# Kernel optimization log

Measured on AMD Instinct MI355X. Metric: run time of the kernel, lower is better.

## Reference

```python
import jax, jax.numpy as jnp
from jax import lax
import numpy as np

DN = ('NDHWC', 'DHWIO', 'NDHWC')

def conv3d(x, w, b, stride=1):
    return lax.conv_general_dilated(x, w, (stride,) * 3, 'SAME', dimension_numbers=DN) + b

def convT3d(x, w, b, stride=2):
    return lax.conv_transpose(x, w, (stride,) * 3, 'SAME', dimension_numbers=DN) + b

def prelu(x, a):
    return jnp.where(x > 0, x, a * x)

def bn(x, g, be, m, v):
    # keras BatchNormalization, inference mode, epsilon=1e-3
    return (x - m) * g * lax.rsqrt(v + 1e-3) + be

def res_unit(x, c1w, c1b, c2w, c2b, g, be, m, v, a):
    # VQVAEResidualUnit: relu(x + PReLU(BN(conv2(swish(conv1(x))))))
    h = jax.nn.swish(conv3d(x, c1w, c1b))
    h = prelu(bn(conv3d(h, c2w, c2b), g, be, m, v), a)
    return jax.nn.relu(x + h)

def _forward(x, ec0_w, ec0_b, er0_c1w, er0_c1b, er0_c2w, er0_c2b, er0_g, er0_be, er0_m, er0_v, er0_a, ec1_w, ec1_b, er1_c1w, er1_c1b, er1_c2w, er1_c2b, er1_g, er1_be, er1_m, er1_v, er1_a, eo_w, eo_b, eo_a, codebook, dc0_w, dc0_b, dc0_a, dr0_c1w, dr0_c1b, dr0_c2w, dr0_c2b, dr0_g, dr0_be, dr0_m, dr0_v, dr0_a, du0_w, du0_b, dr1_c1w, dr1_c1b, dr1_c2w, dr1_c2b, dr1_g, dr1_be, dr1_m, dr1_v, dr1_a, du1_w, du1_b):
    # ----- Encoder -----
    h = jax.nn.relu(conv3d(x, ec0_w, ec0_b, stride=2))   # [B,64,64,64,64]
    h = res_unit(h, er0_c1w, er0_c1b, er0_c2w, er0_c2b, er0_g, er0_be, er0_m, er0_v, er0_a)
    h = jax.nn.relu(conv3d(h, ec1_w, ec1_b, stride=2))   # [B,32,32,32,128]
    h = res_unit(h, er1_c1w, er1_c1b, er1_c2w, er1_c2b, er1_g, er1_be, er1_m, er1_v, er1_a)
    z = prelu(conv3d(h, eo_w, eo_b), eo_a)               # [B,32,32,32,64] latent
    # ----- NSVQ (inference: hard codebook lookup) -----
    D = z.shape[-1]
    flat = z.reshape(-1, D)                              # [N, 64], N = B*32^3
    dist = (flat * flat).sum(1, keepdims=True) + (codebook * codebook).sum(1) - 2.0 * (flat @ codebook.T)  # [N, K]
    idx = jnp.argmin(dist, axis=1)
    zq = codebook[idx].reshape(z.shape)
    K = codebook.shape[0]
    p = jnp.zeros((K,), jnp.float32).at[idx].add(1.0) / flat.shape[0]
    perplexity = jnp.exp(-jnp.sum(p * jnp.log(p + 1e-12)))
    # ----- Decoder -----
    h = prelu(conv3d(zq, dc0_w, dc0_b), dc0_a)           # [B,32,32,32,128]
    h = res_unit(h, dr0_c1w, dr0_c1b, dr0_c2w, dr0_c2b, dr0_g, dr0_be, dr0_m, dr0_v, dr0_a)
    h = jax.nn.relu(convT3d(h, du0_w, du0_b))            # [B,64,64,64,64]
    h = res_unit(h, dr1_c1w, dr1_c1b, dr1_c2w, dr1_c2b, dr1_g, dr1_be, dr1_m, dr1_v, dr1_a)
    recon = convT3d(h, du1_w, du1_b)                     # [B,128,128,128,1]
    return recon, perplexity

def setup_inputs() -> dict:
    key = jax.random.key(0)
    ks = iter(jax.random.split(key, 40))
    nrm = lambda *s: jax.random.normal(next(ks), s, jnp.float32) * 0.05
    def ru(pfx, c):
        return {pfx + '_c1w': nrm(3, 3, 3, c, c), pfx + '_c1b': jnp.zeros((c,), jnp.float32),
                pfx + '_c2w': nrm(3, 3, 3, c, c), pfx + '_c2b': jnp.zeros((c,), jnp.float32),
                pfx + '_g': jnp.ones((c,), jnp.float32), pfx + '_be': jnp.zeros((c,), jnp.float32),
                pfx + '_m': jnp.zeros((c,), jnp.float32), pfx + '_v': jnp.ones((c,), jnp.float32),
                pfx + '_a': jnp.full((c,), 0.25, jnp.float32)}
    C0, C1, D, K = 64, 128, 64, 512
    inp = {'x': jax.random.normal(next(ks), (2, 128, 128, 128, 1), jnp.float32)}
    inp.update(ec0_w=nrm(4, 4, 4, 1, C0), ec0_b=jnp.zeros((C0,), jnp.float32))
    inp.update(ru('er0', C0))
    inp.update(ec1_w=nrm(4, 4, 4, C0, C1), ec1_b=jnp.zeros((C1,), jnp.float32))
    inp.update(ru('er1', C1))
    inp.update(eo_w=nrm(3, 3, 3, C1, D), eo_b=jnp.zeros((D,), jnp.float32), eo_a=jnp.full((D,), 0.25, jnp.float32))
    inp.update(codebook=jax.random.uniform(next(ks), (K, D), jnp.float32, -1.0, 1.0) * np.sqrt(6.0 / D).astype(np.float32))
    inp.update(dc0_w=nrm(3, 3, 3, D, C1), dc0_b=jnp.zeros((C1,), jnp.float32), dc0_a=jnp.full((C1,), 0.25, jnp.float32))
    inp.update(ru('dr0', C1))
    inp.update(du0_w=nrm(4, 4, 4, C1, C0), du0_b=jnp.zeros((C0,), jnp.float32))
    inp.update(ru('dr1', C0))
    inp.update(du1_w=nrm(4, 4, 4, C0, 1), du1_b=jnp.zeros((1,), jnp.float32))
    return inp

def reference(x, ec0_w, ec0_b, er0_c1w, er0_c1b, er0_c2w, er0_c2b, er0_g, er0_be, er0_m, er0_v, er0_a, ec1_w, ec1_b, er1_c1w, er1_c1b, er1_c2w, er1_c2b, er1_g, er1_be, er1_m, er1_v, er1_a, eo_w, eo_b, eo_a, codebook, dc0_w, dc0_b, dc0_a, dr0_c1w, dr0_c1b, dr0_c2w, dr0_c2b, dr0_g, dr0_be, dr0_m, dr0_v, dr0_a, du0_w, du0_b, dr1_c1w, dr1_c1b, dr1_c2w, dr1_c2b, dr1_g, dr1_be, dr1_m, dr1_v, dr1_a, du1_w, du1_b):
    return _forward(x, ec0_w, ec0_b, er0_c1w, er0_c1b, er0_c2w, er0_c2b, er0_g, er0_be, er0_m, er0_v, er0_a, ec1_w, ec1_b, er1_c1w, er1_c1b, er1_c2w, er1_c2b, er1_g, er1_be, er1_m, er1_v, er1_a, eo_w, eo_b, eo_a, codebook, dc0_w, dc0_b, dc0_a, dr0_c1w, dr0_c1b, dr0_c2w, dr0_c2b, dr0_g, dr0_be, dr0_m, dr0_v, dr0_a, du0_w, du0_b, dr1_c1w, dr1_c1b, dr1_c2w, dr1_c2b, dr1_g, dr1_be, dr1_m, dr1_v, dr1_a, du1_w, du1_b)
```

## Files before the change

kernel.cpp:

```cpp
#include <hip/hip_runtime.h>
#include <cstdint>


typedef unsigned short bf16_t;
typedef __attribute__((ext_vector_type(8)))  short s8b;
typedef __attribute__((ext_vector_type(16))) float f32x16;

__device__ __forceinline__ float b2f(bf16_t u) { return __uint_as_float((unsigned)u << 16); }
__device__ __forceinline__ bf16_t f2b(float f) {
    unsigned x = __float_as_uint(f);
    return (bf16_t)((x + 0x7FFFu + ((x >> 16) & 1u)) >> 16);
}

__device__ __forceinline__ void split3s(float v, unsigned short& h,
                                        unsigned short& m, unsigned short& l)
{
    const unsigned uv = __float_as_uint(v);
    const float fh = __uint_as_float(uv & 0xFFFF0000u);
    const float r1 = v - fh;
    const unsigned u1 = __float_as_uint(r1);
    const float fm = __uint_as_float(u1 & 0xFFFF0000u);
    const float r2 = r1 - fm;
    h = (unsigned short)(uv >> 16);
    m = (unsigned short)(u1 >> 16);
    l = (unsigned short)(__float_as_uint(r2) >> 16);
}

__device__ __forceinline__ int wdst(int tap, int ci_, int co_, int ci, int co)
{
    const int ks = ci_ >> 4, half = (ci_ >> 3) & 1, j = ci_ & 7;
    return (((tap * (ci >> 4) + ks) * 2 + half) * co + co_) * 8 + j;
}

__global__ __launch_bounds__(256)
void wprep3(const float* __restrict__ w, bf16_t* __restrict__ h,
            bf16_t* __restrict__ m, bf16_t* __restrict__ l,
            int ci, int co, int n)
{
    const int i = blockIdx.x * 256 + threadIdx.x;
    if (i >= n) return;
    const int co_ = i % co;
    const int ci_ = (i / co) % ci;
    const int tap = i / (co * ci);
    const int dst = wdst(tap, ci_, co_, ci, co);
    unsigned short hh, mm, ll2;
    split3s(w[i], hh, mm, ll2);
    h[dst] = hh; m[dst] = mm; l[dst] = ll2;
}

__global__ __launch_bounds__(256)
void wprep_split(const float* __restrict__ w, bf16_t* __restrict__ hi,
                 bf16_t* __restrict__ lo, int ci, int co, int n)
{
    const int i = blockIdx.x * 256 + threadIdx.x;
    if (i >= n) return;
    const int co_ = i % co;
    const int ci_ = (i / co) % ci;
    const int tap = i / (co * ci);
    const float v = w[i];
    const int dst = wdst(tap, ci_, co_, ci, co);
    const bf16_t h = f2b(v);
    hi[dst] = h;
    lo[dst] = f2b(v - b2f(h));
}

template<int CIN, int COUT, int SD, int NWC, int EPI>
__global__ __launch_bounds__((SD / 32) * NWC * 64)
void conv3e(const float* __restrict__ xf,
            const bf16_t* __restrict__ wh, const bf16_t* __restrict__ wm,
            const bf16_t* __restrict__ wl,
            const float* __restrict__ bias,
            const float* __restrict__ g, const float* __restrict__ be,
            const float* __restrict__ mn, const float* __restrict__ vr,
            const float* __restrict__ al,
            const float* skf, float* __restrict__ of)
{
    constexpr int NT = (SD / 32) * NWC * 64;
    constexpr int LP = (SD * CIN) / (4 * NT);
    constexpr int KS = CIN / 16;
    __shared__ bf16_t lh[(SD + 2) * CIN], lm[(SD + 2) * CIN], ll[(SD + 2) * CIN];

    const int tid  = threadIdx.x;
    const int lane = tid & 63;
    const int wid  = tid >> 6;
    const int wn   = wid % NWC, wm2 = wid / NWC;
    const int half = lane >> 5, ln = lane & 31;
    const int w    = wm2 * 32 + ln;
    const int nwg  = gridDim.x;
    const int bid  = (blockIdx.x & 7) * (nwg >> 3) + (blockIdx.x >> 3);
    const int h    = bid % SD;
    const int d    = (bid / SD) % SD;
    const int b    = bid / (SD * SD);
    const int cout = wn * 32 + ln;

    int pz[9], py[9], pt[9], np = 0;
    for (int kd = 0; kd < 3; ++kd) {
        const int iz = d + kd - 1;
        if ((unsigned)iz >= (unsigned)SD) continue;
        for (int kh = 0; kh < 3; ++kh) {
            const int iy = h + kh - 1;
            if ((unsigned)iy >= (unsigned)SD) continue;
            pz[np] = iz; py[np] = iy; pt[np] = (kd * 3 + kh) * 3; ++np;
        }
    }

    f32x16 accA, accB;
#pragma unroll
    for (int i = 0; i < 16; ++i) { accA[i] = 0.f; accB[i] = 0.f; }

    for (int i = tid; i < CIN / 2; i += NT) {
        const int pv = (i < CIN / 4) ? 0 : (SD + 1);
        const int ch = (i % (CIN / 4)) * 4;
        const int bo = ((pv * CIN + ch) * 2) ^ ((pv & 7) << 4);
        const ushort4 z4 = make_ushort4(0, 0, 0, 0);
        *reinterpret_cast<ushort4*>((char*)&lh[0] + bo) = z4;
        *reinterpret_cast<ushort4*>((char*)&lm[0] + bo) = z4;
        *reinterpret_cast<ushort4*>((char*)&ll[0] + bo) = z4;
    }

    float4 rg[LP];
    auto loadrow = [&](int iz, int iy) {
        const float* src = xf + ((size_t)((b * SD + iz) * SD + iy)) * SD * CIN;
#pragma unroll
        for (int j = 0; j < LP; ++j)
            rg[j] = *reinterpret_cast<const float4*>(src + (size_t)(tid + j * NT) * 4);
    };
    auto writerow = [&]() {
#pragma unroll
        for (int j = 0; j < LP; ++j) {
            const int idx = (tid + j * NT) * 4;
            const int pv = idx / CIN + 1, ch = idx % CIN;
            ushort4 h4, m4, l4;
            split3s(rg[j].x, h4.x, m4.x, l4.x);
            split3s(rg[j].y, h4.y, m4.y, l4.y);
            split3s(rg[j].z, h4.z, m4.z, l4.z);
            split3s(rg[j].w, h4.w, m4.w, l4.w);
            const int bo = ((pv * CIN + ch) * 2) ^ ((pv & 7) << 4);
            *reinterpret_cast<ushort4*>((char*)&lh[0] + bo) = h4;
            *reinterpret_cast<ushort4*>((char*)&lm[0] + bo) = m4;
            *reinterpret_cast<ushort4*>((char*)&ll[0] + bo) = l4;
        }
    };

    loadrow(pz[0], py[0]);
    writerow();
    __syncthreads();
#pragma unroll 1
    for (int i = 0; i < np; ++i) {
        if (i + 1 < np) loadrow(pz[i + 1], py[i + 1]);
#pragma unroll
        for (int kw = 0; kw < 3; ++kw) {
            const int tap = pt[i] + kw;
            const int pv = w + kw;
#pragma unroll
            for (int ks = 0; ks < KS; ++ks) {
                const int bo = ((pv * CIN + half * 8 + ks * 16) * 2) ^ ((pv & 7) << 4);
                const s8b ah  = *reinterpret_cast<const s8b*>((const char*)&lh[0] + bo);
                const s8b am  = *reinterpret_cast<const s8b*>((const char*)&lm[0] + bo);
                const s8b al3 = *reinterpret_cast<const s8b*>((const char*)&ll[0] + bo);
                const size_t wb = ((size_t)((tap * KS + ks) * 2 + half) * COUT + cout) * 8;
                const s8b bh = *reinterpret_cast<const s8b*>(wh + wb);
                const s8b bm = *reinterpret_cast<const s8b*>(wm + wb);
                const s8b bl = *reinterpret_cast<const s8b*>(wl + wb);
                accA = __builtin_amdgcn_mfma_f32_32x32x16_bf16(ah, bh, accA, 0, 0, 0);
                accB = __builtin_amdgcn_mfma_f32_32x32x16_bf16(ah, bm, accB, 0, 0, 0);
                accA = __builtin_amdgcn_mfma_f32_32x32x16_bf16(am, bh, accA, 0, 0, 0);
                accB = __builtin_amdgcn_mfma_f32_32x32x16_bf16(am, bm, accB, 0, 0, 0);
                accA = __builtin_amdgcn_mfma_f32_32x32x16_bf16(al3, bh, accA, 0, 0, 0);
                accB = __builtin_amdgcn_mfma_f32_32x32x16_bf16(ah, bl, accB, 0, 0, 0);
            }
        }
        if (i + 1 < np) {
            __syncthreads();
            writerow();
            __syncthreads();
        }
    }

    const size_t outrow = ((size_t)((b * SD + d) * SD + h)) * SD;
    const float bv = bias[cout];
    float sc = 0.f, mm = 0.f, bb2 = 0.f, aa = 0.f;
    if constexpr (EPI == 3) {
        sc = g[cout] * (1.0f / sqrtf(vr[cout] + 1e-3f));
        mm = mn[cout]; bb2 = be[cout]; aa = al[cout];
    }
    if constexpr (EPI == 2) aa = al[cout];
#pragma unroll
    for (int r = 0; r < 16; ++r) {
        const int rl = (r & 3) + 8 * (r >> 2) + 4 * half;
        const size_t oe = (outrow + wm2 * 32 + rl) * COUT + cout;
        float y = accA[r] + accB[r] + bv;
        if constexpr (EPI == 0) y = fmaxf(y, 0.f);
        else if constexpr (EPI == 1) y = y / (1.f + expf(-y));
        else if constexpr (EPI == 2) y = y > 0.f ? y : aa * y;
        else {
            float t2 = (y - mm) * sc + bb2;
            t2 = t2 > 0.f ? t2 : aa * t2;
            y = fmaxf(skf[oe] + t2, 0.f);
        }
        of[oe] = y;
    }
}

__global__ __launch_bounds__(256)
void convs2e(const float* __restrict__ xf,
             const bf16_t* __restrict__ wh, const bf16_t* __restrict__ wm,
             const bf16_t* __restrict__ wl,
             const float* __restrict__ bias, float* __restrict__ of)
{
    constexpr int NT = 256, LP = (64 * 64) / (4 * NT);
    __shared__ bf16_t lh[66 * 64], lm[66 * 64], ll[66 * 64];

    const int tid  = threadIdx.x;
    const int lane = tid & 63;
    const int wn   = tid >> 6;
    const int half = lane >> 5, ln = lane & 31;
    const int nwg  = gridDim.x;
    const int bid  = (blockIdx.x & 7) * (nwg >> 3) + (blockIdx.x >> 3);
    const int h    = bid % 32;
    const int d    = (bid / 32) % 32;
    const int b    = bid / 1024;
    const int cout = wn * 32 + ln;

    int pz[16], py[16], pt[16], np = 0;
    for (int kd = 0; kd < 4; ++kd) {
        const int iz = 2 * d + kd - 1;
        if ((unsigned)iz >= 64u) continue;
        for (int kh = 0; kh < 4; ++kh) {
            const int iy = 2 * h + kh - 1;
            if ((unsigned)iy >= 64u) continue;
            pz[np] = iz; py[np] = iy; pt[np] = (kd * 4 + kh) * 4; ++np;
        }
    }

    f32x16 accA, accB;
#pragma unroll
    for (int i = 0; i < 16; ++i) { accA[i] = 0.f; accB[i] = 0.f; }

    for (int i = tid; i < 32; i += NT) {
        const int pv = (i < 16) ? 0 : 65;
        const int ch = (i % 16) * 4;
        const int bo = ((pv * 64 + ch) * 2) ^ ((pv & 7) << 4);
        const ushort4 z4 = make_ushort4(0, 0, 0, 0);
        *reinterpret_cast<ushort4*>((char*)&lh[0] + bo) = z4;
        *reinterpret_cast<ushort4*>((char*)&lm[0] + bo) = z4;
        *reinterpret_cast<ushort4*>((char*)&ll[0] + bo) = z4;
    }

    float4 rg[LP];
    auto loadrow = [&](int iz, int iy) {
        const float* src = xf + ((size_t)((b * 64 + iz) * 64 + iy)) * 64 * 64;
#pragma unroll
        for (int j = 0; j < LP; ++j)
            rg[j] = *reinterpret_cast<const float4*>(src + (size_t)(tid + j * NT) * 4);
    };
    auto writerow = [&]() {
#pragma unroll
        for (int j = 0; j < LP; ++j) {
            const int idx = (tid + j * NT) * 4;
            const int pv = idx / 64 + 1, ch = idx % 64;
            ushort4 h4, m4, l4;
            split3s(rg[j].x, h4.x, m4.x, l4.x);
            split3s(rg[j].y, h4.y, m4.y, l4.y);
            split3s(rg[j].z, h4.z, m4.z, l4.z);
            split3s(rg[j].w, h4.w, m4.w, l4.w);
            const int bo = ((pv * 64 + ch) * 2) ^ ((pv & 7) << 4);
            *reinterpret_cast<ushort4*>((char*)&lh[0] + bo) = h4;
            *reinterpret_cast<ushort4*>((char*)&lm[0] + bo) = m4;
            *reinterpret_cast<ushort4*>((char*)&ll[0] + bo) = l4;
        }
    };

    loadrow(pz[0], py[0]);
    writerow();
    __syncthreads();
#pragma unroll 1
    for (int i = 0; i < np; ++i) {
        if (i + 1 < np) loadrow(pz[i + 1], py[i + 1]);
#pragma unroll
        for (int kw = 0; kw < 4; ++kw) {
            const int tap = pt[i] + kw;
            const int pv = 2 * ln + kw;
#pragma unroll
            for (int ks = 0; ks < 4; ++ks) {
                const int bo = ((pv * 64 + half * 8 + ks * 16) * 2) ^ ((pv & 7) << 4);
                const s8b ah  = *reinterpret_cast<const s8b*>((const char*)&lh[0] + bo);
                const s8b am  = *reinterpret_cast<const s8b*>((const char*)&lm[0] + bo);
                const s8b al3 = *reinterpret_cast<const s8b*>((const char*)&ll[0] + bo);
                const size_t wb = ((size_t)((tap * 4 + ks) * 2 + half) * 128 + cout) * 8;
                const s8b bh = *reinterpret_cast<const s8b*>(wh + wb);
                const s8b bm = *reinterpret_cast<const s8b*>(wm + wb);
                const s8b bl = *reinterpret_cast<const s8b*>(wl + wb);
                accA = __builtin_amdgcn_mfma_f32_32x32x16_bf16(ah, bh, accA, 0, 0, 0);
                accB = __builtin_amdgcn_mfma_f32_32x32x16_bf16(ah, bm, accB, 0, 0, 0);
                accA = __builtin_amdgcn_mfma_f32_32x32x16_bf16(am, bh, accA, 0, 0, 0);
                accB = __builtin_amdgcn_mfma_f32_32x32x16_bf16(am, bm, accB, 0, 0, 0);
                accA = __builtin_amdgcn_mfma_f32_32x32x16_bf16(al3, bh, accA, 0, 0, 0);
                accB = __builtin_amdgcn_mfma_f32_32x32x16_bf16(ah, bl, accB, 0, 0, 0);
            }
        }
        if (i + 1 < np) {
            __syncthreads();
            writerow();
            __syncthreads();
        }
    }

    const size_t outrow = ((size_t)((b * 32 + d) * 32 + h)) * 32;
    const float bv = bias[cout];
#pragma unroll
    for (int r = 0; r < 16; ++r) {
        const int rl = (r & 3) + 8 * (r >> 2) + 4 * half;
        const size_t oe = (outrow + rl) * 128 + cout;
        of[oe] = fmaxf(accA[r] + accB[r] + bv, 0.f);
    }
}

template<int CIN, int COUT, int SD, int NWC, int EPI>
__global__ __launch_bounds__((SD / 32) * NWC * 64)
void conv3d(const bf16_t* __restrict__ xh, const bf16_t* __restrict__ xl,
            const bf16_t* __restrict__ wh, const bf16_t* __restrict__ wl,
            const float* __restrict__ bias,
            const float* __restrict__ g, const float* __restrict__ be,
            const float* __restrict__ mn, const float* __restrict__ vr,
            const float* __restrict__ al,
            const bf16_t* skh, const bf16_t* skl,
            bf16_t* oh, bf16_t* ol)
{
    constexpr int NT = (SD / 32) * NWC * 64;
    constexpr int LP = (SD * CIN) / (4 * NT);
    constexpr int KS = CIN / 16;
    __shared__ bf16_t lh[(SD + 2) * CIN], ll[(SD + 2) * CIN];

    const int tid  = threadIdx.x;
    const int lane = tid & 63;
    const int wid  = tid >> 6;
    const int wn   = wid % NWC, wm2 = wid / NWC;
    const int half = lane >> 5, ln = lane & 31;
    const int w    = wm2 * 32 + ln;
    const int nwg  = gridDim.x;
    const int bid  = (blockIdx.x & 7) * (nwg >> 3) + (blockIdx.x >> 3);
    const int h    = bid % SD;
    const int d    = (bid / SD) % SD;
    const int b    = bid / (SD * SD);
    const int cout = wn * 32 + ln;

    int pz[9], py[9], pt[9], np = 0;
    for (int kd = 0; kd < 3; ++kd) {
        const int iz = d + kd - 1;
        if ((unsigned)iz >= (unsigned)SD) continue;
        for (int kh = 0; kh < 3; ++kh) {
            const int iy = h + kh - 1;
            if ((unsigned)iy >= (unsigned)SD) continue;
            pz[np] = iz; py[np] = iy; pt[np] = (kd * 3 + kh) * 3; ++np;
        }
    }

    f32x16 accA, accB;
#pragma unroll
    for (int i = 0; i < 16; ++i) { accA[i] = 0.f; accB[i] = 0.f; }

    for (int i = tid; i < CIN / 2; i += NT) {
        const int pv = (i < CIN / 4) ? 0 : (SD + 1);
        const int ch = (i % (CIN / 4)) * 4;
        const int bo = ((pv * CIN + ch) * 2) ^ ((pv & 7) << 4);
        const ushort4 z4 = make_ushort4(0, 0, 0, 0);
        *reinterpret_cast<ushort4*>((char*)&lh[0] + bo) = z4;
        *reinterpret_cast<ushort4*>((char*)&ll[0] + bo) = z4;
    }

    ushort4 rh[LP], rl2a[LP];
    auto loadrow = [&](int iz, int iy) {
        const size_t rb = ((size_t)((b * SD + iz) * SD + iy)) * SD * CIN;
#pragma unroll
        for (int j = 0; j < LP; ++j) {
            const int idx = (tid + j * NT) * 4;
            rh[j]   = *reinterpret_cast<const ushort4*>(xh + rb + idx);
            rl2a[j] = *reinterpret_cast<const ushort4*>(xl + rb + idx);
        }
    };
    auto writerow = [&]() {
#pragma unroll
        for (int j = 0; j < LP; ++j) {
            const int idx = (tid + j * NT) * 4;
            const int pv = idx / CIN + 1, ch = idx % CIN;
            const int bo = ((pv * CIN + ch) * 2) ^ ((pv & 7) << 4);
            *reinterpret_cast<ushort4*>((char*)&lh[0] + bo) = rh[j];
            *reinterpret_cast<ushort4*>((char*)&ll[0] + bo) = rl2a[j];
        }
    };

    loadrow(pz[0], py[0]);
    writerow();
    __syncthreads();
#pragma unroll 1
    for (int i = 0; i < np; ++i) {
        if (i + 1 < np) loadrow(pz[i + 1], py[i + 1]);
#pragma unroll
        for (int kw = 0; kw < 3; ++kw) {
            const int tap = pt[i] + kw;
            const int pv = w + kw;
#pragma unroll
            for (int ks = 0; ks < KS; ++ks) {
                const int bo = ((pv * CIN + half * 8 + ks * 16) * 2) ^ ((pv & 7) << 4);
                const s8b ah  = *reinterpret_cast<const s8b*>((const char*)&lh[0] + bo);
                const s8b al2 = *reinterpret_cast<const s8b*>((const char*)&ll[0] + bo);
                const size_t wb = ((size_t)((tap * KS + ks) * 2 + half) * COUT + cout) * 8;
                const s8b bh = *reinterpret_cast<const s8b*>(wh + wb);
                const s8b bl = *reinterpret_cast<const s8b*>(wl + wb);
                accA = __builtin_amdgcn_mfma_f32_32x32x16_bf16(ah, bh, accA, 0, 0, 0);
                accB = __builtin_amdgcn_mfma_f32_32x32x16_bf16(al2, bh, accB, 0, 0, 0);
                accB = __builtin_amdgcn_mfma_f32_32x32x16_bf16(ah, bl, accB, 0, 0, 0);
            }
        }
        if (i + 1 < np) {
            __syncthreads();
            writerow();
            __syncthreads();
        }
    }

    const size_t outrow = ((size_t)((b * SD + d) * SD + h)) * SD;
    const float bv = bias[cout];
    float sc = 0.f, mm = 0.f, bb2 = 0.f, aa = 0.f;
    if constexpr (EPI == 3) {
        sc = g[cout] * (1.0f / sqrtf(vr[cout] + 1e-3f));
        mm = mn[cout]; bb2 = be[cout]; aa = al[cout];
    }
    if constexpr (EPI == 2) aa = al[cout];
#pragma unroll
    for (int r = 0; r < 16; ++r) {
        const int rl3 = (r & 3) + 8 * (r >> 2) + 4 * half;
        const size_t oe = (outrow + wm2 * 32 + rl3) * COUT + cout;
        float y = accA[r] + accB[r] + bv;
        if constexpr (EPI == 0) y = fmaxf(y, 0.f);
        else if constexpr (EPI == 1) y = y / (1.f + expf(-y));
        else if constexpr (EPI == 2) y = y > 0.f ? y : aa * y;
        else {
            float t2 = (y - mm) * sc + bb2;
            t2 = t2 > 0.f ? t2 : aa * t2;
            float sv = b2f(skh[oe]) + b2f(skl[oe]);
            y = fmaxf(sv + t2, 0.f);
        }
        const bf16_t hh = f2b(y);
        oh[oe] = hh;
        ol[oe] = f2b(y - b2f(hh));
    }
}

__global__ __launch_bounds__(256)
void convTm(const bf16_t* __restrict__ xh, const bf16_t* __restrict__ xl,
            const bf16_t* __restrict__ wh, const bf16_t* __restrict__ wl,
            const float* __restrict__ bias,
            bf16_t* __restrict__ oh, bf16_t* __restrict__ ol)
{
    constexpr int NT = 256, LP = (32 * 128) / (4 * NT);
    __shared__ bf16_t lh[34 * 128], ll[34 * 128];

    const int tid  = threadIdx.x;
    const int lane = tid & 63;
    const int wid  = tid >> 6;
    const int wn   = wid & 1, p = wid >> 1;
    const int half = lane >> 5, ln = lane & 31;
    const int nwg  = gridDim.x;
    const int bid  = (blockIdx.x & 7) * (nwg >> 3) + (blockIdx.x >> 3);
    const int ohh  = bid % 64;
    const int od   = (bid / 64) % 64;
    const int b    = bid / 4096;
    const int pd = od & 1, dz = od >> 1;
    const int ph = ohh & 1, hy = ohh >> 1;
    const int cout = wn * 32 + ln;

    int pz[4], py[4], pt[4], np = 0;
    for (int jd = 0; jd < 2; ++jd) {
        const int kd = pd + 2 * jd;
        const int iz = dz + pd - 1 + jd;
        if ((unsigned)iz >= 32u) continue;
        for (int jh = 0; jh < 2; ++jh) {
            const int kh = ph + 2 * jh;
            const int iy = hy + ph - 1 + jh;
            if ((unsigned)iy >= 32u) continue;
            pz[np] = iz; py[np] = iy; pt[np] = (kd * 4 + kh) * 4; ++np;
        }
    }

    f32x16 accA, accB;
#pragma unroll
    for (int i = 0; i < 16; ++i) { accA[i] = 0.0f; accB[i] = 0.0f; }

    for (int i = tid; i < 64; i += NT) {
        const int pv = (i < 32) ? 0 : 33;
        const int ch = (i % 32) * 4;
        const int bo = ((pv * 128 + ch) * 2) ^ ((pv & 7) << 4);
        const ushort4 z4 = make_ushort4(0, 0, 0, 0);
        *reinterpret_cast<ushort4*>((char*)&lh[0] + bo) = z4;
        *reinterpret_cast<ushort4*>((char*)&ll[0] + bo) = z4;
    }

    ushort4 rh[LP], rl2a[LP];
    auto loadrow = [&](int iz, int iy) {
        const size_t rb = ((size_t)((b * 32 + iz) * 32 + iy)) * 32 * 128;
#pragma unroll
        for (int j = 0; j < LP; ++j) {
            const int idx = (tid + j * NT) * 4;
            rh[j]   = *reinterpret_cast<const ushort4*>(xh + rb + idx);
            rl2a[j] = *reinterpret_cast<const ushort4*>(xl + rb + idx);
        }
    };
    auto writerow = [&]() {
#pragma unroll
        for (int j = 0; j < LP; ++j) {
            const int idx = (tid + j * NT) * 4;
            const int pv = idx / 128 + 1, ch = idx % 128;
            const int bo = ((pv * 128 + ch) * 2) ^ ((pv & 7) << 4);
            *reinterpret_cast<ushort4*>((char*)&lh[0] + bo) = rh[j];
            *reinterpret_cast<ushort4*>((char*)&ll[0] + bo) = rl2a[j];
        }
    };

    loadrow(pz[0], py[0]);
    writerow();
    __syncthreads();
#pragma unroll 1
    for (int i = 0; i < np; ++i) {
        if (i + 1 < np) loadrow(pz[i + 1], py[i + 1]);
#pragma unroll
        for (int jw = 0; jw < 2; ++jw) {
            const int kw = p + 2 * jw;
            const int tap = pt[i] + kw;
            const int pv = ln + p + jw;
#pragma unroll
            for (int ks = 0; ks < 8; ++ks) {
                const int bo = ((pv * 128 + half * 8 + ks * 16) * 2) ^ ((pv & 7) << 4);
                const s8b a  = *reinterpret_cast<const s8b*>((const char*)&lh[0] + bo);
                const s8b a2 = *reinterpret_cast<const s8b*>((const char*)&ll[0] + bo);
                const size_t wb = ((size_t)((tap * 8 + ks) * 2 + half) * 64 + cout) * 8;
                const s8b bb = *reinterpret_cast<const s8b*>(wh + wb);
                const s8b b2 = *reinterpret_cast<const s8b*>(wl + wb);
                accA = __builtin_amdgcn_mfma_f32_32x32x16_bf16(a, bb, accA, 0, 0, 0);
                accB = __builtin_amdgcn_mfma_f32_32x32x16_bf16(a2, bb, accB, 0, 0, 0);
                accB = __builtin_amdgcn_mfma_f32_32x32x16_bf16(a, b2, accB, 0, 0, 0);
            }
        }
        if (i + 1 < np) {
            __syncthreads();
            writerow();
            __syncthreads();
        }
    }

    const float bv = bias[cout];
#pragma unroll
    for (int r = 0; r < 16; ++r) {
        const int rl3 = (r & 3) + 8 * (r >> 2) + 4 * half;
        const int ow = 2 * rl3 + p;
        const size_t oe = (((size_t)((b * 64 + od) * 64 + ohh)) * 64 + ow) * 64 + cout;
        const float y = fmaxf(accA[r] + accB[r] + bv, 0.f);
        const bf16_t hh = f2b(y);
        oh[oe] = hh;
        ol[oe] = f2b(y - b2f(hh));
    }
}

__global__ __launch_bounds__(128)
void conv_ec0m(const float* __restrict__ x,
               const bf16_t* __restrict__ wh, const bf16_t* __restrict__ wm,
               const bf16_t* __restrict__ wl,
               const float* __restrict__ bias, float* __restrict__ of)
{
    __shared__ bf16_t lh[16 * 132], lm[16 * 132], ll[16 * 132];

    const int tid  = threadIdx.x;
    const int lane = tid & 63;
    const int wm2  = tid >> 6;
    const int half = lane >> 5, ln = lane & 31;
    const int w    = wm2 * 32 + ln;
    const int nwg  = gridDim.x;
    const int bid  = (blockIdx.x & 7) * (nwg >> 3) + (blockIdx.x >> 3);
    const int h    = bid % 64;
    const int d    = (bid / 64) % 64;
    const int b    = bid / 4096;

    for (int i = tid; i < 16 * 132; i += 128) {
        const int row = i / 132, col = i % 132;
        const int kd = row >> 2, kh = row & 3;
        const int iz = 2 * d + kd - 1, iy = 2 * h + kh - 1;
        const int ix = col - 1;
        float v = 0.f;
        if ((unsigned)iz < 128u && (unsigned)iy < 128u &&
            (unsigned)ix < 128u && col < 130)
            v = x[(size_t)((b * 128 + iz) * 128 + iy) * 128 + ix];
        unsigned short hh, mm2, ll2;
        split3s(v, hh, mm2, ll2);
        lh[i] = hh; lm[i] = mm2; ll[i] = ll2;
    }
    __syncthreads();

    f32x16 accA[2], accB[2];
#pragma unroll
    for (int i = 0; i < 16; ++i) {
        accA[0][i] = 0.f; accA[1][i] = 0.f;
        accB[0][i] = 0.f; accB[1][i] = 0.f;
    }

#pragma unroll
    for (int ks = 0; ks < 4; ++ks) {
        const int row0 = ks * 4 + 2 * half;
        const int i0 = row0 * 132 + 2 * w;
        const int i1 = i0 + 132;
        s8b ah, am, al3;
        {
            uint* ap = (uint*)&ah;
            ap[0] = *(const uint*)&lh[i0]; ap[1] = *(const uint*)&lh[i0 + 2];
            ap[2] = *(const uint*)&lh[i1]; ap[3] = *(const uint*)&lh[i1 + 2];
        }
        {
            uint* ap = (uint*)&am;
            ap[0] = *(const uint*)&lm[i0]; ap[1] = *(const uint*)&lm[i0 + 2];
            ap[2] = *(const uint*)&lm[i1]; ap[3] = *(const uint*)&lm[i1 + 2];
        }
        {
            uint* ap = (uint*)&al3;
            ap[0] = *(const uint*)&ll[i0]; ap[1] = *(const uint*)&ll[i0 + 2];
            ap[2] = *(const uint*)&ll[i1]; ap[3] = *(const uint*)&ll[i1 + 2];
        }
        const size_t wb0 = ((size_t)(ks * 2 + half) * 64 + ln) * 8;
#pragma unroll
        for (int n2 = 0; n2 < 2; ++n2) {
            const size_t wb = wb0 + n2 * 256;
            const s8b bh = *reinterpret_cast<const s8b*>(wh + wb);
            const s8b bm = *reinterpret_cast<const s8b*>(wm + wb);
            const s8b bl = *reinterpret_cast<const s8b*>(wl + wb);
            accA[n2] = __builtin_amdgcn_mfma_f32_32x32x16_bf16(ah, bh, accA[n2], 0, 0, 0);
            accB[n2] = __builtin_amdgcn_mfma_f32_32x32x16_bf16(ah, bm, accB[n2], 0, 0, 0);
            accA[n2] = __builtin_amdgcn_mfma_f32_32x32x16_bf16(am, bh, accA[n2], 0, 0, 0);
            accB[n2] = __builtin_amdgcn_mfma_f32_32x32x16_bf16(am, bm, accB[n2], 0, 0, 0);
            accA[n2] = __builtin_amdgcn_mfma_f32_32x32x16_bf16(al3, bh, accA[n2], 0, 0, 0);
            accB[n2] = __builtin_amdgcn_mfma_f32_32x32x16_bf16(ah, bl, accB[n2], 0, 0, 0);
        }
    }

    const size_t outrow = ((size_t)((b * 64 + d) * 64 + h)) * 64;
#pragma unroll
    for (int n2 = 0; n2 < 2; ++n2) {
        const int cout = n2 * 32 + ln;
        const float bv = bias[cout];
#pragma unroll
        for (int r = 0; r < 16; ++r) {
            const int rl3 = (r & 3) + 8 * (r >> 2) + 4 * half;
            const size_t oe = (outrow + wm2 * 32 + rl3) * 64 + cout;
            of[oe] = fmaxf(accA[n2][r] + accB[n2][r] + bv, 0.f);
        }
    }
}

__global__ __launch_bounds__(256)
void convT_du1w(const bf16_t* __restrict__ inh, const bf16_t* __restrict__ inl,
                const float* __restrict__ wt, const float* __restrict__ bias,
                float* __restrict__ out)
{
    const int lane = threadIdx.x & 63;
    const int wv   = blockIdx.x * 4 + (threadIdx.x >> 6);
    const size_t obase = (size_t)wv * 16;
    const int ow0 = (int)(obase % 128);
    size_t rem = obase / 128;
    const int ohh = (int)(rem % 128); rem /= 128;
    const int od  = (int)(rem % 128); rem /= 128;
    const int b   = (int)rem;
    const int pd = od & 1, dz = od >> 1;
    const int ph = ohh & 1, hy = ohh >> 1;
    const int wx0 = ow0 >> 1;

    float acc[16];
#pragma unroll
    for (int o = 0; o < 16; ++o) acc[o] = 0.f;

#pragma unroll
    for (int jd = 0; jd < 2; ++jd) {
        const int kd = pd + 2 * jd;
        const int iz = dz + pd - 1 + jd;
        if ((unsigned)iz >= 64u) continue;
#pragma unroll
        for (int jh = 0; jh < 2; ++jh) {
            const int kh = ph + 2 * jh;
            const int iy = hy + ph - 1 + jh;
            if ((unsigned)iy >= 64u) continue;
            const size_t rbase = ((size_t)((b * 64 + iz) * 64 + iy)) * 64;
            float wv4[4];
#pragma unroll
            for (int kw = 0; kw < 4; ++kw)
                wv4[kw] = wt[(size_t)((kd * 4 + kh) * 4 + kw) * 64 + lane];
            float v[10];
#pragma unroll
            for (int t = 0; t < 10; ++t) {
                const int ix = wx0 - 1 + t;
                if ((unsigned)ix < 64u) {
                    const size_t a = (rbase + ix) * 64 + lane;
                    v[t] = b2f(inh[a]) + b2f(inl[a]);
                } else {
                    v[t] = 0.f;
                }
            }
#pragma unroll
            for (int o = 0; o < 16; ++o) {
                const int pw = o & 1;
                const int t0 = (o >> 1) + pw;
                acc[o] = fmaf(v[t0],     wv4[pw],     acc[o]);
                acc[o] = fmaf(v[t0 + 1], wv4[pw + 2], acc[o]);
            }
        }
    }

    const float b0 = bias[0];
#pragma unroll
    for (int o = 0; o < 16; ++o) {
        float s = acc[o];
        s += __shfl_xor(s, 1);
        s += __shfl_xor(s, 2);
        s += __shfl_xor(s, 4);
        s += __shfl_xor(s, 8);
        s += __shfl_xor(s, 16);
        s += __shfl_xor(s, 32);
        if (lane == 0) out[obase + o] = s + b0;
    }
}

__global__ void zero512(float* __restrict__ p) { p[threadIdx.x] = 0.0f; }

__global__ void vq_cnorm(const float* __restrict__ cb, float* __restrict__ cnorm)
{
    const int k = blockIdx.x * 64 + threadIdx.x;
    float s = 0.0f;
    for (int ci = 0; ci < 64; ++ci) { const float c = cb[k * 64 + ci]; s = fmaf(c, c, s); }
    cnorm[k] = s;
}

__global__ __launch_bounds__(256)
void vq_assign(const float* __restrict__ z, const float* __restrict__ cb,
               const float* __restrict__ cnorm, int* __restrict__ idx,
               float* __restrict__ hist, int N)
{
    const int n = blockIdx.x * 256 + threadIdx.x;
    const float4* zp = reinterpret_cast<const float4*>(z + (size_t)n * 64);
    float4 zv[16];
    float z2 = 0.0f;
#pragma unroll
    for (int i = 0; i < 16; ++i) {
        zv[i] = zp[i];
        z2 += zv[i].x * zv[i].x + zv[i].y * zv[i].y + zv[i].z * zv[i].z + zv[i].w * zv[i].w;
    }
    float best = 3.4e38f;
    int bi = 0;
#pragma unroll 1
    for (int k = 0; k < 512; k += 4) {
        float dot0 = 0.f, dot1 = 0.f, dot2 = 0.f, dot3 = 0.f;
        const float4* c0 = reinterpret_cast<const float4*>(cb + (size_t)(k + 0) * 64);
        const float4* c1 = reinterpret_cast<const float4*>(cb + (size_t)(k + 1) * 64);
        const float4* c2 = reinterpret_cast<const float4*>(cb + (size_t)(k + 2) * 64);
        const float4* c3 = reinterpret_cast<const float4*>(cb + (size_t)(k + 3) * 64);
#pragma unroll
        for (int i = 0; i < 16; ++i) {
            const float4 zi = zv[i];
            const float4 a0 = c0[i];
            const float4 a1 = c1[i];
            const float4 a2 = c2[i];
            const float4 a3 = c3[i];
            dot0 += zi.x * a0.x + zi.y * a0.y + zi.z * a0.z + zi.w * a0.w;
            dot1 += zi.x * a1.x + zi.y * a1.y + zi.z * a1.z + zi.w * a1.w;
            dot2 += zi.x * a2.x + zi.y * a2.y + zi.z * a2.z + zi.w * a2.w;
            dot3 += zi.x * a3.x + zi.y * a3.y + zi.z * a3.z + zi.w * a3.w;
        }
        const float d0 = z2 + cnorm[k + 0] - 2.0f * dot0;
        const float d1 = z2 + cnorm[k + 1] - 2.0f * dot1;
        const float d2 = z2 + cnorm[k + 2] - 2.0f * dot2;
        const float d3 = z2 + cnorm[k + 3] - 2.0f * dot3;
        if (d0 < best) { best = d0; bi = k + 0; }
        if (d1 < best) { best = d1; bi = k + 1; }
        if (d2 < best) { best = d2; bi = k + 2; }
        if (d3 < best) { best = d3; bi = k + 3; }
    }
    idx[n] = bi;
    atomicAdd(&hist[bi], 1.0f);
}

__global__ __launch_bounds__(256)
void vq_gather_split(const float* __restrict__ cb, const int* __restrict__ idx,
                     bf16_t* __restrict__ zh, bf16_t* __restrict__ zl)
{
    const int gid = blockIdx.x * 256 + threadIdx.x;
    const int n = gid >> 4, c4 = gid & 15;
    const int k = idx[n];
    const float4 c = reinterpret_cast<const float4*>(cb)[k * 16 + c4];
    ushort4 h, l;
    h.x = f2b(c.x); l.x = f2b(c.x - b2f(h.x));
    h.y = f2b(c.y); l.y = f2b(c.y - b2f(h.y));
    h.z = f2b(c.z); l.z = f2b(c.z - b2f(h.z));
    h.w = f2b(c.w); l.w = f2b(c.w - b2f(h.w));
    reinterpret_cast<ushort4*>(zh)[gid] = h;
    reinterpret_cast<ushort4*>(zl)[gid] = l;
}

__global__ __launch_bounds__(512)
void perplexity_k(const float* __restrict__ hist, float* __restrict__ out, float invN)
{
    __shared__ float red[512];
    const int t = threadIdx.x;
    const float p = hist[t] * invN;
    red[t] = p * logf(p + 1e-12f);
    __syncthreads();
    for (int s = 256; s > 0; s >>= 1) {
        if (t < s) red[t] += red[t + s];
        __syncthreads();
    }
    if (t == 0) out[0] = expf(-red[0]);
}

extern "C" void kernel_launch(void* const* d_in, const int* in_sizes, int n_in,
                              void* d_out, int out_size, void* d_ws, size_t ws_size,
                              hipStream_t stream)
{
    const float* x       = (const float*)d_in[0];
    const float* ec0_w   = (const float*)d_in[1];
    const float* ec0_b   = (const float*)d_in[2];
    const float* er0_c1w = (const float*)d_in[3];
    const float* er0_c1b = (const float*)d_in[4];
    const float* er0_c2w = (const float*)d_in[5];
    const float* er0_c2b = (const float*)d_in[6];
    const float* er0_g   = (const float*)d_in[7];
    const float* er0_be  = (const float*)d_in[8];
    const float* er0_m   = (const float*)d_in[9];
    const float* er0_v   = (const float*)d_in[10];
    const float* er0_a   = (const float*)d_in[11];
    const float* ec1_w   = (const float*)d_in[12];
    const float* ec1_b   = (const float*)d_in[13];
    const float* er1_c1w = (const float*)d_in[14];
    const float* er1_c1b = (const float*)d_in[15];
    const float* er1_c2w = (const float*)d_in[16];
    const float* er1_c2b = (const float*)d_in[17];
    const float* er1_g   = (const float*)d_in[18];
    const float* er1_be  = (const float*)d_in[19];
    const float* er1_m   = (const float*)d_in[20];
    const float* er1_v   = (const float*)d_in[21];
    const float* er1_a   = (const float*)d_in[22];
    const float* eo_w    = (const float*)d_in[23];
    const float* eo_b    = (const float*)d_in[24];
    const float* eo_a    = (const float*)d_in[25];
    const float* cb      = (const float*)d_in[26];
    const float* dc0_w   = (const float*)d_in[27];
    const float* dc0_b   = (const float*)d_in[28];
    const float* dc0_a   = (const float*)d_in[29];
    const float* dr0_c1w = (const float*)d_in[30];
// ... 139 lines not shown
```

Before: 5.177 ms.

## Double-buffer LDS input rows in conv kernels to drop one barrier per tap

Each conv kernel now keeps two LDS row buffers. The next row is split and written into the idle buffer while the MFMA loop reads the current one, and the following row's global load is issued two steps ahead. This replaces the two barriers and serialized write per tap with a single barrier, so the split/write overlaps with matrix work. In exchange LDS use doubles and more registers stay live, which may reduce occupancy.

```diff
diff --git a/kernel.cpp b/kernel.cpp
--- a/kernel.cpp
+++ b/kernel.cpp
@@ -78,7 +78,8 @@
     constexpr int NT = (SD / 32) * NWC * 64;
     constexpr int LP = (SD * CIN) / (4 * NT);
     constexpr int KS = CIN / 16;
-    __shared__ bf16_t lh[(SD + 2) * CIN], lm[(SD + 2) * CIN], ll[(SD + 2) * CIN];
+    constexpr int RB = (SD + 2) * CIN;
+    __shared__ bf16_t lh[2][RB], lm[2][RB], ll[2][RB];
 
     const int tid  = threadIdx.x;
     const int lane = tid & 63;
@@ -108,14 +109,16 @@
 #pragma unroll
     for (int i = 0; i < 16; ++i) { accA[i] = 0.f; accB[i] = 0.f; }
 
-    for (int i = tid; i < CIN / 2; i += NT) {
-        const int pv = (i < CIN / 4) ? 0 : (SD + 1);
-        const int ch = (i % (CIN / 4)) * 4;
+    for (int i = tid; i < CIN; i += NT) {
+        const int bf2 = i / (CIN / 2);
+        const int rem = i % (CIN / 2);
+        const int pv = (rem < CIN / 4) ? 0 : (SD + 1);
+        const int ch = (rem % (CIN / 4)) * 4;
         const int bo = ((pv * CIN + ch) * 2) ^ ((pv & 7) << 4);
         const ushort4 z4 = make_ushort4(0, 0, 0, 0);
-        *reinterpret_cast<ushort4*>((char*)&lh[0] + bo) = z4;
-        *reinterpret_cast<ushort4*>((char*)&lm[0] + bo) = z4;
-        *reinterpret_cast<ushort4*>((char*)&ll[0] + bo) = z4;
+        *reinterpret_cast<ushort4*>((char*)&lh[bf2][0] + bo) = z4;
+        *reinterpret_cast<ushort4*>((char*)&lm[bf2][0] + bo) = z4;
+        *reinterpret_cast<ushort4*>((char*)&ll[bf2][0] + bo) = z4;
     }
 
     float4 rg[LP];
@@ -125,7 +128,7 @@
         for (int j = 0; j < LP; ++j)
             rg[j] = *reinterpret_cast<const float4*>(src + (size_t)(tid + j * NT) * 4);
     };
-    auto writerow = [&]() {
+    auto writerow = [&](int bf2) {
 #pragma unroll
         for (int j = 0; j < LP; ++j) {
             const int idx = (tid + j * NT) * 4;
@@ -136,18 +139,21 @@
             split3s(rg[j].z, h4.z, m4.z, l4.z);
             split3s(rg[j].w, h4.w, m4.w, l4.w);
             const int bo = ((pv * CIN + ch) * 2) ^ ((pv & 7) << 4);
-            *reinterpret_cast<ushort4*>((char*)&lh[0] + bo) = h4;
-            *reinterpret_cast<ushort4*>((char*)&lm[0] + bo) = m4;
-            *reinterpret_cast<ushort4*>((char*)&ll[0] + bo) = l4;
+            *reinterpret_cast<ushort4*>((char*)&lh[bf2][0] + bo) = h4;
+            *reinterpret_cast<ushort4*>((char*)&lm[bf2][0] + bo) = m4;
+            *reinterpret_cast<ushort4*>((char*)&ll[bf2][0] + bo) = l4;
         }
     };
 
     loadrow(pz[0], py[0]);
-    writerow();
+    writerow(0);
+    if (np > 1) loadrow(pz[1], py[1]);
     __syncthreads();
 #pragma unroll 1
     for (int i = 0; i < np; ++i) {
-        if (i + 1 < np) loadrow(pz[i + 1], py[i + 1]);
+        const int cur = i & 1;
+        if (i + 1 < np) writerow((i + 1) & 1);
+        if (i + 2 < np) loadrow(pz[i + 2], py[i + 2]);
 #pragma unroll
         for (int kw = 0; kw < 3; ++kw) {
             const int tap = pt[i] + kw;
@@ -155,9 +161,9 @@
 #pragma unroll
             for (int ks = 0; ks < KS; ++ks) {
                 const int bo = ((pv * CIN + half * 8 + ks * 16) * 2) ^ ((pv & 7) << 4);
-                const s8b ah  = *reinterpret_cast<const s8b*>((const char*)&lh[0] + bo);
-                const s8b am  = *reinterpret_cast<const s8b*>((const char*)&lm[0] + bo);
-                const s8b al3 = *reinterpret_cast<const s8b*>((const char*)&ll[0] + bo);
+                const s8b ah  = *reinterpret_cast<const s8b*>((const char*)&lh[cur][0] + bo);
+                const s8b am  = *reinterpret_cast<const s8b*>((const char*)&lm[cur][0] + bo);
+                const s8b al3 = *reinterpret_cast<const s8b*>((const char*)&ll[cur][0] + bo);
                 const size_t wb = ((size_t)((tap * KS + ks) * 2 + half) * COUT + cout) * 8;
                 const s8b bh = *reinterpret_cast<const s8b*>(wh + wb);
                 const s8b bm = *reinterpret_cast<const s8b*>(wm + wb);
@@ -170,11 +176,7 @@
                 accB = __builtin_amdgcn_mfma_f32_32x32x16_bf16(ah, bl, accB, 0, 0, 0);
             }
         }
-        if (i + 1 < np) {
-            __syncthreads();
-            writerow();
-            __syncthreads();
-        }
+        __syncthreads();
     }
 
     const size_t outrow = ((size_t)((b * SD + d) * SD + h)) * SD;
@@ -209,7 +211,7 @@
              const float* __restrict__ bias, float* __restrict__ of)
 {
     constexpr int NT = 256, LP = (64 * 64) / (4 * NT);
-    __shared__ bf16_t lh[66 * 64], lm[66 * 64], ll[66 * 64];
+    __shared__ bf16_t lh[2][66 * 64], lm[2][66 * 64], ll[2][66 * 64];
 
     const int tid  = threadIdx.x;
     const int lane = tid & 63;
@@ -237,14 +239,16 @@
 #pragma unroll
     for (int i = 0; i < 16; ++i) { accA[i] = 0.f; accB[i] = 0.f; }
 
-    for (int i = tid; i < 32; i += NT) {
-        const int pv = (i < 16) ? 0 : 65;
-        const int ch = (i % 16) * 4;
+    for (int i = tid; i < 64; i += NT) {
+        const int bf2 = i / 32;
+        const int rem = i % 32;
+        const int pv = (rem < 16) ? 0 : 65;
+        const int ch = (rem % 16) * 4;
         const int bo = ((pv * 64 + ch) * 2) ^ ((pv & 7) << 4);
         const ushort4 z4 = make_ushort4(0, 0, 0, 0);
-        *reinterpret_cast<ushort4*>((char*)&lh[0] + bo) = z4;
-        *reinterpret_cast<ushort4*>((char*)&lm[0] + bo) = z4;
-        *reinterpret_cast<ushort4*>((char*)&ll[0] + bo) = z4;
+        *reinterpret_cast<ushort4*>((char*)&lh[bf2][0] + bo) = z4;
+        *reinterpret_cast<ushort4*>((char*)&lm[bf2][0] + bo) = z4;
+        *reinterpret_cast<ushort4*>((char*)&ll[bf2][0] + bo) = z4;
     }
 
     float4 rg[LP];
@@ -254,7 +258,7 @@
         for (int j = 0; j < LP; ++j)
             rg[j] = *reinterpret_cast<const float4*>(src + (size_t)(tid + j * NT) * 4);
     };
-    auto writerow = [&]() {
+    auto writerow = [&](int bf2) {
 #pragma unroll
         for (int j = 0; j < LP; ++j) {
             const int idx = (tid + j * NT) * 4;
@@ -265,18 +269,21 @@
             split3s(rg[j].z, h4.z, m4.z, l4.z);
             split3s(rg[j].w, h4.w, m4.w, l4.w);
             const int bo = ((pv * 64 + ch) * 2) ^ ((pv & 7) << 4);
-            *reinterpret_cast<ushort4*>((char*)&lh[0] + bo) = h4;
-            *reinterpret_cast<ushort4*>((char*)&lm[0] + bo) = m4;
-            *reinterpret_cast<ushort4*>((char*)&ll[0] + bo) = l4;
+            *reinterpret_cast<ushort4*>((char*)&lh[bf2][0] + bo) = h4;
+            *reinterpret_cast<ushort4*>((char*)&lm[bf2][0] + bo) = m4;
+            *reinterpret_cast<ushort4*>((char*)&ll[bf2][0] + bo) = l4;
         }
     };
 
     loadrow(pz[0], py[0]);
-    writerow();
+    writerow(0);
+    if (np > 1) loadrow(pz[1], py[1]);
     __syncthreads();
 #pragma unroll 1
     for (int i = 0; i < np; ++i) {
-        if (i + 1 < np) loadrow(pz[i + 1], py[i + 1]);
+        const int cur = i & 1;
+        if (i + 1 < np) writerow((i + 1) & 1);
+        if (i + 2 < np) loadrow(pz[i + 2], py[i + 2]);
 #pragma unroll
         for (int kw = 0; kw < 4; ++kw) {
             const int tap = pt[i] + kw;
@@ -284,9 +291,9 @@
 #pragma unroll
             for (int ks = 0; ks < 4; ++ks) {
                 const int bo = ((pv * 64 + half * 8 + ks * 16) * 2) ^ ((pv & 7) << 4);
-                const s8b ah  = *reinterpret_cast<const s8b*>((const char*)&lh[0] + bo);
-                const s8b am  = *reinterpret_cast<const s8b*>((const char*)&lm[0] + bo);
-                const s8b al3 = *reinterpret_cast<const s8b*>((const char*)&ll[0] + bo);
+                const s8b ah  = *reinterpret_cast<const s8b*>((const char*)&lh[cur][0] + bo);
+                const s8b am  = *reinterpret_cast<const s8b*>((const char*)&lm[cur][0] + bo);
+                const s8b al3 = *reinterpret_cast<const s8b*>((const char*)&ll[cur][0] + bo);
                 const size_t wb = ((size_t)((tap * 4 + ks) * 2 + half) * 128 + cout) * 8;
                 const s8b bh = *reinterpret_cast<const s8b*>(wh + wb);
                 const s8b bm = *reinterpret_cast<const s8b*>(wm + wb);
@@ -299,11 +306,7 @@
                 accB = __builtin_amdgcn_mfma_f32_32x32x16_bf16(ah, bl, accB, 0, 0, 0);
             }
         }
-        if (i + 1 < np) {
-            __syncthreads();
-            writerow();
-            __syncthreads();
-        }
+        __syncthreads();
     }
 
     const size_t outrow = ((size_t)((b * 32 + d) * 32 + h)) * 32;
@@ -330,7 +333,8 @@
     constexpr int NT = (SD / 32) * NWC * 64;
     constexpr int LP = (SD * CIN) / (4 * NT);
     constexpr int KS = CIN / 16;
-    __shared__ bf16_t lh[(SD + 2) * CIN], ll[(SD + 2) * CIN];
+    constexpr int RB = (SD + 2) * CIN;
+    __shared__ bf16_t lh[2][RB], ll[2][RB];
 
     const int tid  = threadIdx.x;
     const int lane = tid & 63;
@@ -360,13 +364,15 @@
 #pragma unroll
     for (int i = 0; i < 16; ++i) { accA[i] = 0.f; accB[i] = 0.f; }
 
-    for (int i = tid; i < CIN / 2; i += NT) {
-        const int pv = (i < CIN / 4) ? 0 : (SD + 1);
-        const int ch = (i % (CIN / 4)) * 4;
+    for (int i = tid; i < CIN; i += NT) {
+        const int bf2 = i / (CIN / 2);
+        const int rem = i % (CIN / 2);
+        const int pv = (rem < CIN / 4) ? 0 : (SD + 1);
+        const int ch = (rem % (CIN / 4)) * 4;
         const int bo = ((pv * CIN + ch) * 2) ^ ((pv & 7) << 4);
         const ushort4 z4 = make_ushort4(0, 0, 0, 0);
-        *reinterpret_cast<ushort4*>((char*)&lh[0] + bo) = z4;
-        *reinterpret_cast<ushort4*>((char*)&ll[0] + bo) = z4;
+        *reinterpret_cast<ushort4*>((char*)&lh[bf2][0] + bo) = z4;
+        *reinterpret_cast<ushort4*>((char*)&ll[bf2][0] + bo) = z4;
     }
 
     ushort4 rh[LP], rl2a[LP];
@@ -379,23 +385,26 @@
             rl2a[j] = *reinterpret_cast<const ushort4*>(xl + rb + idx);
         }
     };
-    auto writerow = [&]() {
+    auto writerow = [&](int bf2) {
 #pragma unroll
         for (int j = 0; j < LP; ++j) {
             const int idx = (tid + j * NT) * 4;
             const int pv = idx / CIN + 1, ch = idx % CIN;
             const int bo = ((pv * CIN + ch) * 2) ^ ((pv & 7) << 4);
-            *reinterpret_cast<ushort4*>((char*)&lh[0] + bo) = rh[j];
-            *reinterpret_cast<ushort4*>((char*)&ll[0] + bo) = rl2a[j];
+            *reinterpret_cast<ushort4*>((char*)&lh[bf2][0] + bo) = rh[j];
+            *reinterpret_cast<ushort4*>((char*)&ll[bf2][0] + bo) = rl2a[j];
         }
     };
 
     loadrow(pz[0], py[0]);
-    writerow();
+    writerow(0);
+    if (np > 1) loadrow(pz[1], py[1]);
     __syncthreads();
 #pragma unroll 1
     for (int i = 0; i < np; ++i) {
-        if (i + 1 < np) loadrow(pz[i + 1], py[i + 1]);
+        const int cur = i & 1;
+        if (i + 1 < np) writerow((i + 1) & 1);
+        if (i + 2 < np) loadrow(pz[i + 2], py[i + 2]);
 #pragma unroll
         for (int kw = 0; kw < 3; ++kw) {
             const int tap = pt[i] + kw;
@@ -403,8 +412,8 @@
 #pragma unroll
             for (int ks = 0; ks < KS; ++ks) {
                 const int bo = ((pv * CIN + half * 8 + ks * 16) * 2) ^ ((pv & 7) << 4);
-                const s8b ah  = *reinterpret_cast<const s8b*>((const char*)&lh[0] + bo);
-                const s8b al2 = *reinterpret_cast<const s8b*>((const char*)&ll[0] + bo);
+                const s8b ah  = *reinterpret_cast<const s8b*>((const char*)&lh[cur][0] + bo);
+                const s8b al2 = *reinterpret_cast<const s8b*>((const char*)&ll[cur][0] + bo);
                 const size_t wb = ((size_t)((tap * KS + ks) * 2 + half) * COUT + cout) * 8;
                 const s8b bh = *reinterpret_cast<const s8b*>(wh + wb);
                 const s8b bl = *reinterpret_cast<const s8b*>(wl + wb);
@@ -413,11 +422,7 @@
                 accB = __builtin_amdgcn_mfma_f32_32x32x16_bf16(ah, bl, accB, 0, 0, 0);
             }
         }
-        if (i + 1 < np) {
-            __syncthreads();
-            writerow();
-            __syncthreads();
-        }
+        __syncthreads();
     }
 
     const size_t outrow = ((size_t)((b * SD + d) * SD + h)) * SD;
@@ -455,7 +460,7 @@
             bf16_t* __restrict__ oh, bf16_t* __restrict__ ol)
 {
     constexpr int NT = 256, LP = (32 * 128) / (4 * NT);
-    __shared__ bf16_t lh[34 * 128], ll[34 * 128];
+    __shared__ bf16_t lh[2][34 * 128], ll[2][34 * 128];
 
     const int tid  = threadIdx.x;
     const int lane = tid & 63;
@@ -488,13 +493,15 @@
 #pragma unroll
     for (int i = 0; i < 16; ++i) { accA[i] = 0.0f; accB[i] = 0.0f; }
 
-    for (int i = tid; i < 64; i += NT) {
-        const int pv = (i < 32) ? 0 : 33;
-        const int ch = (i % 32) * 4;
+    for (int i = tid; i < 128; i += NT) {
+        const int bf2 = i / 64;
+        const int rem = i % 64;
+        const int pv = (rem < 32) ? 0 : 33;
+        const int ch = (rem % 32) * 4;
         const int bo = ((pv * 128 + ch) * 2) ^ ((pv & 7) << 4);
         const ushort4 z4 = make_ushort4(0, 0, 0, 0);
-        *reinterpret_cast<ushort4*>((char*)&lh[0] + bo) = z4;
-        *reinterpret_cast<ushort4*>((char*)&ll[0] + bo) = z4;
+        *reinterpret_cast<ushort4*>((char*)&lh[bf2][0] + bo) = z4;
+        *reinterpret_cast<ushort4*>((char*)&ll[bf2][0] + bo) = z4;
     }
 
     ushort4 rh[LP], rl2a[LP];
@@ -507,23 +514,26 @@
             rl2a[j] = *reinterpret_cast<const ushort4*>(xl + rb + idx);
         }
     };
-    auto writerow = [&]() {
+    auto writerow = [&](int bf2) {
 #pragma unroll
         for (int j = 0; j < LP; ++j) {
             const int idx = (tid + j * NT) * 4;
             const int pv = idx / 128 + 1, ch = idx % 128;
             const int bo = ((pv * 128 + ch) * 2) ^ ((pv & 7) << 4);
-            *reinterpret_cast<ushort4*>((char*)&lh[0] + bo) = rh[j];
-            *reinterpret_cast<ushort4*>((char*)&ll[0] + bo) = rl2a[j];
+            *reinterpret_cast<ushort4*>((char*)&lh[bf2][0] + bo) = rh[j];
+            *reinterpret_cast<ushort4*>((char*)&ll[bf2][0] + bo) = rl2a[j];
         }
     };
 
     loadrow(pz[0], py[0]);
-    writerow();
+    writerow(0);
+    if (np > 1) loadrow(pz[1], py[1]);
     __syncthreads();
 #pragma unroll 1
     for (int i = 0; i < np; ++i) {
-        if (i + 1 < np) loadrow(pz[i + 1], py[i + 1]);
+        const int cur = i & 1;
+        if (i + 1 < np) writerow((i + 1) & 1);
+        if (i + 2 < np) loadrow(pz[i + 2], py[i + 2]);
 #pragma unroll
         for (int jw = 0; jw < 2; ++jw) {
             const int kw = p + 2 * jw;
@@ -532,8 +542,8 @@
 #pragma unroll
             for (int ks = 0; ks < 8; ++ks) {
                 const int bo = ((pv * 128 + half * 8 + ks * 16) * 2) ^ ((pv & 7) << 4);
-                const s8b a  = *reinterpret_cast<const s8b*>((const char*)&lh[0] + bo);
-                const s8b a2 = *reinterpret_cast<const s8b*>((const char*)&ll[0] + bo);
+                const s8b a  = *reinterpret_cast<const s8b*>((const char*)&lh[cur][0] + bo);
+                const s8b a2 = *reinterpret_cast<const s8b*>((const char*)&ll[cur][0] + bo);
                 const size_t wb = ((size_t)((tap * 8 + ks) * 2 + half) * 64 + cout) * 8;
                 const s8b bb = *reinterpret_cast<const s8b*>(wh + wb);
                 const s8b b2 = *reinterpret_cast<const s8b*>(wl + wb);
@@ -542,11 +552,7 @@
                 accB = __builtin_amdgcn_mfma_f32_32x32x16_bf16(a, b2, accB, 0, 0, 0);
             }
         }
-        if (i + 1 < np) {
-            __syncthreads();
-            writerow();
-            __syncthreads();
-        }
+        __syncthreads();
     }
 
     const float bv = bias[cout];
```

Result: no change. 5.127 ms (-1.0%).
